# Performance work log

Measured on AMD Instinct MI355X. Metric: run time of the kernel, lower is better.

## Reference

```python
import jax, jax.numpy as jnp
import numpy as np

B, S, D = 2, 2048, 1024
H, KH = 16, 4            # query heads, kv heads
DK = D // H              # 64
REP = H // KH            # queries per kv head


def _rope(x):
    # x: (B, h, S, dk); non-interleaved rotate-half RoPE as in source
    dk = x.shape[-1]
    half = dk // 2
    seq = x.shape[2]
    theta = 10000.0 ** (-(jnp.arange(half, dtype=jnp.float32) / half))
    pos = jnp.arange(seq, dtype=jnp.float32)
    freqs = pos[:, None] * theta[None, :]          # (S, half)
    cos = jnp.cos(freqs)[None, None]               # (1,1,S,half)
    sin = jnp.sin(freqs)[None, None]
    x1, x2 = x[..., :half], x[..., half:]
    return jnp.concatenate([x1 * cos - x2 * sin, x2 * cos + x1 * sin], axis=-1)


def setup_inputs() -> dict:
    key = jax.random.key(0)
    ks = jax.random.split(key, 9)
    sd = 1.0 / np.sqrt(D)
    x = jax.random.normal(ks[0], (B, S, D), dtype=jnp.float32)
    # causal mask: 1 where attend allowed, 0 where masked (mask==0 -> -inf)
    mask = jnp.tril(jnp.ones((S, S), dtype=jnp.int32))[None, None]
    Wq = jax.random.normal(ks[1], (D, H * DK), dtype=jnp.float32) * sd
    bq = jnp.zeros((H * DK,), dtype=jnp.float32)
    Wk = jax.random.normal(ks[2], (D, KH * DK), dtype=jnp.float32) * sd
    bk = jnp.zeros((KH * DK,), dtype=jnp.float32)
    Wv = jax.random.normal(ks[3], (D, KH * DK), dtype=jnp.float32) * sd
    bv = jnp.zeros((KH * DK,), dtype=jnp.float32)
    Wo = jax.random.normal(ks[4], (H * DK, D), dtype=jnp.float32) * sd
    bo = jnp.zeros((D,), dtype=jnp.float32)
    return {"x": x, "mask": mask, "Wq": Wq, "bq": bq, "Wk": Wk, "bk": bk,
            "Wv": Wv, "bv": bv, "Wo": Wo, "bo": bo}


def reference(x, mask, Wq, bq, Wk, bk, Wv, bv, Wo, bo):
    b, s, _ = x.shape
    q = (x @ Wq + bq).reshape(b, s, H, DK).transpose(0, 2, 1, 3)   # (B,H,S,DK)
    k = (x @ Wk + bk).reshape(b, s, KH, DK).transpose(0, 2, 1, 3)  # (B,KH,S,DK)
    v = (x @ Wv + bv).reshape(b, s, KH, DK).transpose(0, 2, 1, 3)
    q = _rope(q)
    k = _rope(k)
    k = jnp.repeat(k, REP, axis=1)  # GQA expand: (B,H,S,DK)
    v = jnp.repeat(v, REP, axis=1)
    attn = jnp.einsum('bhqd,bhkd->bhqk', q, k) / np.sqrt(DK).astype(np.float32)
    attn = jnp.where(mask == 0, -jnp.inf, attn)
    score = jax.nn.softmax(attn, axis=-1)
    out = jnp.einsum('bhqk,bhkd->bhqd', score, v)   # (B,H,S,DK)
    out = out.transpose(0, 2, 1, 3).reshape(b, s, H * DK)
    return out @ Wo + bo
```

## Files before the change

kernel.cpp:

```cpp
#include <hip/hip_runtime.h>
#include <math.h>

#define B_   2
#define S_   2048
#define D_   1024
#define H_   16
#define KH_  4
#define DK_  64

using bf16x8 = __attribute__((ext_vector_type(8))) short;
using bf16x4 = __attribute__((ext_vector_type(4))) short;
using f32x4  = __attribute__((ext_vector_type(4))) float;
using u32x4  = __attribute__((ext_vector_type(4))) unsigned int;
using u32x2  = __attribute__((ext_vector_type(2))) unsigned int;

__device__ inline unsigned short f2bf(float f) {
    unsigned u = __float_as_uint(f);
    u += 0x7FFFu + ((u >> 16) & 1u);
    return (unsigned short)(u >> 16);
}
__device__ inline float bf2f(unsigned short u) {
    return __uint_as_float(((unsigned)u) << 16);
}

#ifdef __has_builtin
#if __has_builtin(__builtin_amdgcn_cvt_pk_bf16_f32)
#define PKBF16 1
#endif
#endif
__device__ inline unsigned pk2bf(float a, float b) {
#ifdef PKBF16
    auto r = __builtin_amdgcn_cvt_pk_bf16_f32(a, b);
    unsigned u; __builtin_memcpy(&u, &r, 4);
    return u;
#else
    return (unsigned)f2bf(a) | ((unsigned)f2bf(b) << 16);
#endif
}

#define GL16(gp, lp) __builtin_amdgcn_global_load_lds( \
    (const __attribute__((address_space(1))) unsigned int*)(gp), \
    (__attribute__((address_space(3))) unsigned int*)(lp), 16, 0, 0)

__global__ __launch_bounds__(256) void prep_kernel(
    const float* __restrict__ x,
    const float* __restrict__ Wq, const float* __restrict__ Wk,
    const float* __restrict__ Wv, const float* __restrict__ Wo,
    unsigned short* __restrict__ xb,
    unsigned short* __restrict__ WqkvT,
    unsigned short* __restrict__ WoT)
{
    __shared__ float T[64][65];
    const int t = threadIdx.x;
    int bx = blockIdx.x;

    if (bx < 2048) {
        const int i = bx * 256 + t;
        f32x4 a = *(const f32x4*)(x + (long)i * 8);
        f32x4 b = *(const f32x4*)(x + (long)i * 8 + 4);
        bf16x8 o;
        o[0] = (short)f2bf(a[0]); o[1] = (short)f2bf(a[1]);
        o[2] = (short)f2bf(a[2]); o[3] = (short)f2bf(a[3]);
        o[4] = (short)f2bf(b[0]); o[5] = (short)f2bf(b[1]);
        o[6] = (short)f2bf(b[2]); o[7] = (short)f2bf(b[3]);
        *(bf16x8*)(xb + (long)i * 8) = o;
        return;
    }
    bx -= 2048;
    const float* in; unsigned short* out; int C;
    if (bx < 256)      { in = Wq; out = WqkvT;               C = 1024; }
    else if (bx < 320) { in = Wk; out = WqkvT + 1024 * 1024; C = 256;  bx -= 256; }
    else if (bx < 384) { in = Wv; out = WqkvT + 1280 * 1024; C = 256;  bx -= 320; }
    else               { in = Wo; out = WoT;                 C = 1024; bx -= 384; }
    const int R  = 1024, nr = 16;
    const int r0 = (bx % nr) * 64;
    const int c0 = (bx / nr) * 64;
    {
        const int r  = t >> 2;
        const int cq = (t & 3) * 16;
        const float* src = in + (long)(r0 + r) * C + c0 + cq;
        #pragma unroll
        for (int i = 0; i < 4; ++i) {
            f32x4 v = *(const f32x4*)(src + i * 4);
            T[r][cq + i * 4 + 0] = v[0];
            T[r][cq + i * 4 + 1] = v[1];
            T[r][cq + i * 4 + 2] = v[2];
            T[r][cq + i * 4 + 3] = v[3];
        }
    }
    __syncthreads();
    {
        const int c  = t >> 2;
        const int rq = (t & 3) * 16;
        bf16x8 p0, p1;
        #pragma unroll
        for (int i = 0; i < 8; ++i) {
            p0[i] = (short)f2bf(T[rq + i][c]);
            p1[i] = (short)f2bf(T[rq + 8 + i][c]);
        }
        unsigned short* dst = out + (long)(c0 + c) * R + r0 + rq;
        *(bf16x8*)dst       = p0;
        *(bf16x8*)(dst + 8) = p1;
    }
}

template<bool BF16OUT>
__global__ __launch_bounds__(256) void gemm64_kernel(
    const unsigned short* __restrict__ A,
    const unsigned short* __restrict__ Bt,
    const float* __restrict__ b0,
    const float* __restrict__ b1,
    const float* __restrict__ b2,
    float* __restrict__ outf,
    unsigned short* __restrict__ outb,
    int N, int K)
{
    __shared__ unsigned short As[2][64][32];
    __shared__ unsigned short Bs[2][128][32];

    const int t  = threadIdx.x;
    const int m0 = blockIdx.x * 64;
    const int n0 = blockIdx.y * 128;

    const int w    = t >> 6;
    const int lane = t & 63;
    const int n    = lane & 15;
    const int quad = lane >> 4;
    const int wm   = (w >> 1) * 32;
    const int wn   = (w & 1) * 64;

    const int lr4 = lane >> 2;
    const int cs  = ((lane & 3) ^ (lr4 & 3)) * 8;

    const unsigned short* gA  = A  + (long)(m0 + w * 16 + lr4) * K + cs;
    const unsigned short* gB0 = Bt + (long)(n0 + w * 32 + lr4) * K + cs;
    const unsigned short* gB1 = gB0 + (long)16 * K;

    GL16(gA,  &As[0][w * 16][0]);
    GL16(gB0, &Bs[0][w * 32][0]);
    GL16(gB1, &Bs[0][w * 32 + 16][0]);

    f32x4 acc[2][4];
    #pragma unroll
    for (int i = 0; i < 2; ++i)
        #pragma unroll
        for (int j = 0; j < 4; ++j) acc[i][j] = 0.0f;

    const int cr = (quad ^ (n & 3)) * 8;

    for (int k0 = 0; k0 < K; k0 += 32) {
        const int cur = (k0 >> 5) & 1;
        __syncthreads();
        if (k0 + 32 < K) {
            const int nb = cur ^ 1;
            GL16(gA  + k0 + 32, &As[nb][w * 16][0]);
            GL16(gB0 + k0 + 32, &Bs[nb][w * 32][0]);
            GL16(gB1 + k0 + 32, &Bs[nb][w * 32 + 16][0]);
        }

        bf16x8 af[2], bfr[4];
        #pragma unroll
        for (int i = 0; i < 2; ++i)
            af[i] = *(const bf16x8*)&As[cur][wm + i * 16 + n][cr];
        #pragma unroll
        for (int j = 0; j < 4; ++j)
            bfr[j] = *(const bf16x8*)&Bs[cur][wn + j * 16 + n][cr];
        #pragma unroll
        for (int mi = 0; mi < 2; ++mi)
            #pragma unroll
            for (int ni = 0; ni < 4; ++ni)
                acc[mi][ni] = __builtin_amdgcn_mfma_f32_16x16x32_bf16(
                    af[mi], bfr[ni], acc[mi][ni], 0, 0, 0);
    }

    #pragma unroll
    for (int mi = 0; mi < 2; ++mi) {
        #pragma unroll
        for (int r = 0; r < 4; ++r) {
            const int gm = m0 + wm + mi * 16 + quad * 4 + r;
            #pragma unroll
            for (int ni = 0; ni < 4; ++ni) {
                const int gn = n0 + wn + ni * 16 + n;
                if (BF16OUT) {
                    const float b = (gn < 1024) ? b0[gn]
                                  : (gn < 1280) ? b1[gn - 1024]
                                                : b2[gn - 1280];
                    outb[(long)gm * N + gn] = f2bf(acc[mi][ni][r] + b);
                } else {
                    outf[(long)gm * N + gn] = acc[mi][ni][r] + b0[gn];
                }
            }
        }
    }
}

__global__ __launch_bounds__(256) void scatter_kernel(
    const unsigned short* __restrict__ qkvm,
    unsigned short* __restrict__ qbuf,
    unsigned short* __restrict__ kbuf,
    unsigned short* __restrict__ vbuf)
{
    __shared__ unsigned short T[64][72];
    const int t = threadIdx.x;
    int bx = blockIdx.x;

    if (bx < 1280) {
        const int idx = bx * 256 + t;
        const int m   = idx / 80;
        const int rem = idx - m * 80;
        const int h20 = rem >> 2;
        const int d0  = (rem & 3) * 8;

        const int s  = m & (S_ - 1);
        const int bb = m >> 11;
        const int col0 = (h20 < 16) ? h20 * 64 + d0 : 1024 + (h20 - 16) * 64 + d0;
        const float scl = (h20 < 16) ? 0.1803368801111606f : 1.0f;

        const bf16x8 x1v = *(const bf16x8*)(qkvm + (long)m * 1536 + col0);
        const bf16x8 x2v = *(const bf16x8*)(qkvm + (long)m * 1536 + col0 + 32);
        bf16x8 o1, o2;
        #pragma unroll
        for (int j = 0; j < 8; ++j) {
            const int d = d0 + j;
            const float theta = exp2f(-(float)d * (13.287712379549449f / 32.0f));
            const float f = (float)s * theta;
            const float c = cosf(f) * scl, sn = sinf(f) * scl;
            const float x1 = bf2f((unsigned short)x1v[j]);
            const float x2 = bf2f((unsigned short)x2v[j]);
            o1[j] = (short)f2bf(x1 * c - x2 * sn);
            o2[j] = (short)f2bf(x2 * c + x1 * sn);
        }
        unsigned short* dst = (h20 < 16)
            ? qbuf + ((long)(bb * H_ + h20) * S_ + s) * DK_ + d0
            : kbuf + ((long)(bb * KH_ + (h20 - 16)) * S_ + s) * DK_ + d0;
        *(bf16x8*)dst        = o1;
        *(bf16x8*)(dst + 32) = o2;
        return;
    }
    bx -= 1280;
    const int bkh = bx >> 5;
    const int s0  = (bx & 31) * 64;
    {
        const int s  = t >> 2;
        const int dq = (t & 3) * 16;
        const unsigned short* src =
            qkvm + (long)((bkh >> 2) * S_ + s0 + s) * 1536 + 1280 + (bkh & 3) * 64 + dq;
        *(bf16x8*)&T[s][dq]     = *(const bf16x8*)src;
        *(bf16x8*)&T[s][dq + 8] = *(const bf16x8*)(src + 8);
    }
    __syncthreads();
    {
        const int d  = t >> 2;
        const int sq = (t & 3) * 16;
        bf16x8 p0, p1;
        #pragma unroll
        for (int i = 0; i < 8; ++i) {
            p0[i] = (short)T[sq + i][d];
            p1[i] = (short)T[sq + 8 + i][d];
        }
        unsigned short* dst = vbuf + ((long)bkh * DK_ + d) * S_ + s0 + sq;
        *(bf16x8*)dst       = p0;
        *(bf16x8*)(dst + 8) = p1;
    }
}

__global__ __launch_bounds__(256) void attn_kernel(
    const unsigned short* __restrict__ qb,
    const unsigned short* __restrict__ kbf,
    const unsigned short* __restrict__ vT,
    unsigned short* __restrict__ ot)
{
    __shared__ unsigned short Ks[2][64][80];
    __shared__ unsigned short Vs[2][64][80];
    __shared__ unsigned short Ps[4][16][80];

    const int tid = threadIdx.x;
    const int bx  = blockIdx.x;
    const int qt  = 31 - (bx >> 5);
    const int bh  = bx & 31;
    const int b   = bh >> 4, h = bh & 15;
    const int kh  = h >> 2;
    const int q0  = qt * 64;

    const int wv   = tid >> 6;
    const int lane = tid & 63;
    const int n    = lane & 15;
    const int quad = lane >> 4;

    const unsigned short* qp =
        qb + ((long)(b * H_ + h) * S_ + q0 + wv * 16 + n) * DK_;
    const bf16x8 qa0 = *(const bf16x8*)(qp + quad * 8);
    const bf16x8 qa1 = *(const bf16x8*)(qp + 32 + quad * 8);

    f32x4 O[4];
    #pragma unroll
    for (int dt = 0; dt < 4; ++dt) O[dt] = 0.0f;
    float lsum = 0.f;

    const unsigned short* kbase = kbf + (long)(b * KH_ + kh) * S_ * DK_;
    const unsigned short* vbase = vT  + (long)(b * KH_ + kh) * DK_ * S_;

    const int ntiles = qt + 1;
    const int srow = tid >> 3;
    const int sc8  = (tid & 7) * 8;

    u32x4 kr0 = *(const u32x4*)(kbase + (long)srow * DK_ + sc8);
    u32x4 kr1 = *(const u32x4*)(kbase + (long)(32 + srow) * DK_ + sc8);
    u32x4 vr0 = *(const u32x4*)(vbase + (long)srow * S_ + sc8);
    u32x4 vr1 = *(const u32x4*)(vbase + (long)(32 + srow) * S_ + sc8);
    *(u32x4*)&Ks[0][srow][sc8]      = kr0;
    *(u32x4*)&Ks[0][32 + srow][sc8] = kr1;
    *(u32x4*)&Vs[0][srow][sc8]      = vr0;
    *(u32x4*)&Vs[0][32 + srow][sc8] = vr1;

    for (int u = 0; u < ntiles; ++u) {
        const int cur = u & 1;
        const int kb  = u * 64;
        __syncthreads();

        if (u + 1 < ntiles) {
            const int kbn = kb + 64;
            kr0 = *(const u32x4*)(kbase + (long)(kbn + srow) * DK_ + sc8);
            kr1 = *(const u32x4*)(kbase + (long)(kbn + 32 + srow) * DK_ + sc8);
            vr0 = *(const u32x4*)(vbase + (long)srow * S_ + kbn + sc8);
            vr1 = *(const u32x4*)(vbase + (long)(32 + srow) * S_ + kbn + sc8);
        }

        f32x4 sc[4];
        #pragma unroll
        for (int ct = 0; ct < 4; ++ct) {
            const bf16x8 kf0 = *(const bf16x8*)&Ks[cur][ct * 16 + n][quad * 8];
            const bf16x8 kf1 = *(const bf16x8*)&Ks[cur][ct * 16 + n][32 + quad * 8];
            f32x4 c = 0.0f;
            c = __builtin_amdgcn_mfma_f32_16x16x32_bf16(kf0, qa0, c, 0, 0, 0);
            c = __builtin_amdgcn_mfma_f32_16x16x32_bf16(kf1, qa1, c, 0, 0, 0);
            sc[ct] = c;
        }

        if (u == qt) {
            const int qg = q0 + wv * 16 + n;
            #pragma unroll
            for (int ct = 0; ct < 4; ++ct) {
                const int kq = kb + ct * 16 + quad * 4;
                #pragma unroll
                for (int r = 0; r < 4; ++r)
                    if (kq + r > qg) sc[ct][r] = -INFINITY;
            }
        }
        f32x4 rs4 = 0.0f;
        #pragma unroll
        for (int ct = 0; ct < 4; ++ct) {
            #pragma unroll
            for (int r = 0; r < 4; ++r) {
                const float p = exp2f(sc[ct][r]);
                sc[ct][r] = p;
                rs4[r] += p;
            }
        }
        lsum += (rs4[0] + rs4[1]) + (rs4[2] + rs4[3]);

        #pragma unroll
        for (int ct = 0; ct < 4; ++ct) {
            u32x2 pw;
            pw[0] = pk2bf(sc[ct][0], sc[ct][1]);
            pw[1] = pk2bf(sc[ct][2], sc[ct][3]);
            *(u32x2*)&Ps[wv][n][ct * 16 + quad * 4] = pw;
        }
        const bf16x8 pb0 = *(const bf16x8*)&Ps[wv][n][quad * 8];
        const bf16x8 pb1 = *(const bf16x8*)&Ps[wv][n][32 + quad * 8];

        #pragma unroll
        for (int dt = 0; dt < 4; ++dt) {
            const bf16x8 av0 = *(const bf16x8*)&Vs[cur][dt * 16 + n][quad * 8];
            const bf16x8 av1 = *(const bf16x8*)&Vs[cur][dt * 16 + n][32 + quad * 8];
            O[dt] = __builtin_amdgcn_mfma_f32_16x16x32_bf16(av0, pb0, O[dt], 0, 0, 0);
            O[dt] = __builtin_amdgcn_mfma_f32_16x16x32_bf16(av1, pb1, O[dt], 0, 0, 0);
        }

        if (u + 1 < ntiles) {
            const int nb = cur ^ 1;
            *(u32x4*)&Ks[nb][srow][sc8]      = kr0;
            *(u32x4*)&Ks[nb][32 + srow][sc8] = kr1;
            *(u32x4*)&Vs[nb][srow][sc8]      = vr0;
            *(u32x4*)&Vs[nb][32 + srow][sc8] = vr1;
        }
    }

    lsum += __shfl_xor(lsum, 16);
    lsum += __shfl_xor(lsum, 32);
    const float inv = 1.0f / lsum;
    #pragma unroll
    for (int dt = 0; dt < 4; ++dt) {
        u32x2 pw;
        pw[0] = pk2bf(O[dt][0] * inv, O[dt][1] * inv);
        pw[1] = pk2bf(O[dt][2] * inv, O[dt][3] * inv);
        *(u32x2*)&Ps[wv][n][dt * 16 + quad * 4] = pw;
    }
    const int fr = lane >> 3;
    const int c8 = (lane & 7) * 8;
    #pragma unroll
    for (int it = 0; it < 2; ++it) {
        const int row = it * 8 + fr;
        const int q   = q0 + wv * 16 + row;
        unsigned short* op = ot + ((long)(b * S_ + q) * H_ + h) * DK_ + c8;
        *(bf16x8*)op = *(const bf16x8*)&Ps[wv][row][c8];
    }
}

extern "C" void kernel_launch(void* const* d_in, const int* in_sizes, int n_in,
                              void* d_out, int out_size, void* d_ws, size_t ws_size,
                              hipStream_t stream)
{
    const float* x  = (const float*)d_in[0];
    const float* Wq = (const float*)d_in[2];
    const float* bq = (const float*)d_in[3];
    const float* Wk = (const float*)d_in[4];
    const float* bk = (const float*)d_in[5];
    const float* Wv = (const float*)d_in[6];
    const float* bv = (const float*)d_in[7];
    const float* Wo = (const float*)d_in[8];
    const float* bo = (const float*)d_in[9];
    float* out = (float*)d_out;

    unsigned short* ws    = (unsigned short*)d_ws;
    unsigned short* xb    = ws;
    unsigned short* qkvm  = xb + 4194304;
    unsigned short* qbuf  = qkvm + 6291456;
    unsigned short* kbuf  = qbuf + 4194304;
    unsigned short* vbuf  = kbuf + 1048576;
    unsigned short* WqkvT = vbuf + 1048576;
    unsigned short* WoT   = WqkvT + 1572864;
    unsigned short* ob    = qkvm;

    prep_kernel<<<2688, 256, 0, stream>>>(x, Wq, Wk, Wv, Wo, xb, WqkvT, WoT);

    gemm64_kernel<true><<<dim3(64, 12), 256, 0, stream>>>(
        xb, WqkvT, bq, bk, bv, nullptr, qkvm, 1536, 1024);

    scatter_kernel<<<1536, 256, 0, stream>>>(qkvm, qbuf, kbuf, vbuf);

    attn_kernel<<<B_ * H_ * (S_ / 64), 256, 0, stream>>>(qbuf, kbuf, vbuf, ob);

    gemm64_kernel<false><<<dim3(64, 8), 256, 0, stream>>>(
        ob, WoT, bo, nullptr, nullptr, out, nullptr, 1024, 1024);
}
```

Before: 192.6 us.

## XOR-swizzle attention LDS tiles, reorder block schedule, raise MFMA wave priority

Replaces the padded 80-wide LDS rows for K, V and P with unpadded 64-wide rows that use an XOR swizzle of the 16-byte column chunk by row. This is meant to avoid bank conflicts while cutting shared memory per block. It also remaps block indices so that each wave of 256 blocks mixes long and short causal query tiles, aiming to balance load across CUs. It wraps the MFMA sections in s_setprio to favour matrix-issuing waves. Every writer and reader must agree on the swizzle index math, which adds some ALU work.

```diff
diff --git a/kernel.cpp b/kernel.cpp
--- a/kernel.cpp
+++ b/kernel.cpp
@@ -270,14 +270,23 @@
     const unsigned short* __restrict__ vT,
     unsigned short* __restrict__ ot)
 {
-    __shared__ unsigned short Ks[2][64][80];
-    __shared__ unsigned short Vs[2][64][80];
-    __shared__ unsigned short Ps[4][16][80];
+    __shared__ __align__(16) unsigned short Ks[2][64][64];
+    __shared__ __align__(16) unsigned short Vs[2][64][64];
+    __shared__ __align__(16) unsigned short Ps[4][16][64];
 
     const int tid = threadIdx.x;
     const int bx  = blockIdx.x;
-    const int qt  = 31 - (bx >> 5);
-    const int bh  = bx & 31;
+
+    const int g = bx >> 8;
+    const int p = bx & 255;
+    const int a = p >> 4;
+    int qt;
+    if      (g == 0) qt = 31 - a;
+    else if (g == 1) qt = a;
+    else if (g == 2) qt = 16 + a;
+    else             qt = 15 - a;
+    const int bh = (p & 15) | ((g & 2) << 3);
+
     const int b   = bh >> 4, h = bh & 15;
     const int kh  = h >> 2;
     const int q0  = qt * 64;
@@ -286,6 +295,7 @@
     const int lane = tid & 63;
     const int n    = lane & 15;
     const int quad = lane >> 4;
+    const int xk   = n & 7;
 
     const unsigned short* qp =
         qb + ((long)(b * H_ + h) * S_ + q0 + wv * 16 + n) * DK_;
@@ -302,16 +312,18 @@
 
     const int ntiles = qt + 1;
     const int srow = tid >> 3;
-    const int sc8  = (tid & 7) * 8;
+    const int lc   = tid & 7;
+    const int sc8  = lc * 8;
+    const int pcs  = (lc ^ (srow & 7)) * 8;
 
     u32x4 kr0 = *(const u32x4*)(kbase + (long)srow * DK_ + sc8);
     u32x4 kr1 = *(const u32x4*)(kbase + (long)(32 + srow) * DK_ + sc8);
     u32x4 vr0 = *(const u32x4*)(vbase + (long)srow * S_ + sc8);
     u32x4 vr1 = *(const u32x4*)(vbase + (long)(32 + srow) * S_ + sc8);
-    *(u32x4*)&Ks[0][srow][sc8]      = kr0;
-    *(u32x4*)&Ks[0][32 + srow][sc8] = kr1;
-    *(u32x4*)&Vs[0][srow][sc8]      = vr0;
-    *(u32x4*)&Vs[0][32 + srow][sc8] = vr1;
+    *(u32x4*)&Ks[0][srow][pcs]      = kr0;
+    *(u32x4*)&Ks[0][32 + srow][pcs] = kr1;
+    *(u32x4*)&Vs[0][srow][pcs]      = vr0;
+    *(u32x4*)&Vs[0][32 + srow][pcs] = vr1;
 
     for (int u = 0; u < ntiles; ++u) {
         const int cur = u & 1;
@@ -327,15 +339,19 @@
         }
 
         f32x4 sc[4];
+        __builtin_amdgcn_s_setprio(1);
         #pragma unroll
         for (int ct = 0; ct < 4; ++ct) {
-            const bf16x8 kf0 = *(const bf16x8*)&Ks[cur][ct * 16 + n][quad * 8];
-            const bf16x8 kf1 = *(const bf16x8*)&Ks[cur][ct * 16 + n][32 + quad * 8];
+            const bf16x8 kf0 =
+                *(const bf16x8*)&Ks[cur][ct * 16 + n][(quad ^ xk) * 8];
+            const bf16x8 kf1 =
+                *(const bf16x8*)&Ks[cur][ct * 16 + n][((quad + 4) ^ xk) * 8];
             f32x4 c = 0.0f;
             c = __builtin_amdgcn_mfma_f32_16x16x32_bf16(kf0, qa0, c, 0, 0, 0);
             c = __builtin_amdgcn_mfma_f32_16x16x32_bf16(kf1, qa1, c, 0, 0, 0);
             sc[ct] = c;
         }
+        __builtin_amdgcn_s_setprio(0);
 
         if (u == qt) {
             const int qg = q0 + wv * 16 + n;
@@ -364,25 +380,30 @@
             u32x2 pw;
             pw[0] = pk2bf(sc[ct][0], sc[ct][1]);
             pw[1] = pk2bf(sc[ct][2], sc[ct][3]);
-            *(u32x2*)&Ps[wv][n][ct * 16 + quad * 4] = pw;
-        }
-        const bf16x8 pb0 = *(const bf16x8*)&Ps[wv][n][quad * 8];
-        const bf16x8 pb1 = *(const bf16x8*)&Ps[wv][n][32 + quad * 8];
-
+            const int pc = ((2 * ct + (quad >> 1)) ^ xk) * 8 + (quad & 1) * 4;
+            *(u32x2*)&Ps[wv][n][pc] = pw;
+        }
+        const bf16x8 pb0 = *(const bf16x8*)&Ps[wv][n][(quad ^ xk) * 8];
+        const bf16x8 pb1 = *(const bf16x8*)&Ps[wv][n][((quad + 4) ^ xk) * 8];
+
+        __builtin_amdgcn_s_setprio(1);
         #pragma unroll
         for (int dt = 0; dt < 4; ++dt) {
-            const bf16x8 av0 = *(const bf16x8*)&Vs[cur][dt * 16 + n][quad * 8];
-            const bf16x8 av1 = *(const bf16x8*)&Vs[cur][dt * 16 + n][32 + quad * 8];
+            const bf16x8 av0 =
+                *(const bf16x8*)&Vs[cur][dt * 16 + n][(quad ^ xk) * 8];
+            const bf16x8 av1 =
+                *(const bf16x8*)&Vs[cur][dt * 16 + n][((quad + 4) ^ xk) * 8];
             O[dt] = __builtin_amdgcn_mfma_f32_16x16x32_bf16(av0, pb0, O[dt], 0, 0, 0);
             O[dt] = __builtin_amdgcn_mfma_f32_16x16x32_bf16(av1, pb1, O[dt], 0, 0, 0);
         }
+        __builtin_amdgcn_s_setprio(0);
 
         if (u + 1 < ntiles) {
             const int nb = cur ^ 1;
-            *(u32x4*)&Ks[nb][srow][sc8]      = kr0;
-            *(u32x4*)&Ks[nb][32 + srow][sc8] = kr1;
-            *(u32x4*)&Vs[nb][srow][sc8]      = vr0;
-            *(u32x4*)&Vs[nb][32 + srow][sc8] = vr1;
+            *(u32x4*)&Ks[nb][srow][pcs]      = kr0;
+            *(u32x4*)&Ks[nb][32 + srow][pcs] = kr1;
+            *(u32x4*)&Vs[nb][srow][pcs]      = vr0;
+            *(u32x4*)&Vs[nb][32 + srow][pcs] = vr1;
         }
     }
 
@@ -394,16 +415,17 @@
         u32x2 pw;
         pw[0] = pk2bf(O[dt][0] * inv, O[dt][1] * inv);
         pw[1] = pk2bf(O[dt][2] * inv, O[dt][3] * inv);
-        *(u32x2*)&Ps[wv][n][dt * 16 + quad * 4] = pw;
+        const int pc = ((2 * dt + (quad >> 1)) ^ xk) * 8 + (quad & 1) * 4;
+        *(u32x2*)&Ps[wv][n][pc] = pw;
     }
     const int fr = lane >> 3;
-    const int c8 = (lane & 7) * 8;
+    const int c8l = lane & 7;
     #pragma unroll
     for (int it = 0; it < 2; ++it) {
         const int row = it * 8 + fr;
         const int q   = q0 + wv * 16 + row;
-        unsigned short* op = ot + ((long)(b * S_ + q) * H_ + h) * DK_ + c8;
-        *(bf16x8*)op = *(const bf16x8*)&Ps[wv][row][c8];
+        unsigned short* op = ot + ((long)(b * S_ + q) * H_ + h) * DK_ + c8l * 8;
+        *(bf16x8*)op = *(const bf16x8*)&Ps[wv][row][(c8l ^ fr) * 8];
     }
 }
 
```

Measured after the change: 195.6 us. Within noise of the previous version (+1.6%).
